# Kernel optimization log

Measured on AMD Instinct MI355X. Metric: run time of the kernel, lower is better.

Reference implementation:

```python
import jax, jax.numpy as jnp
import numpy as np

TEMPERATURE = 0.1
EPS_NORM = 1e-12  # torch F.normalize eps
EPS_LOSS = 1e-8


def setup_inputs() -> dict:
    key = jax.random.key(0)
    k1, k2 = jax.random.split(key)
    N, D, K = 8192, 512, 64
    features = jax.random.normal(k1, (N, D), dtype=jnp.float32)
    cluster_assignments = jax.random.randint(k2, (N,), 0, K, dtype=jnp.int64)
    return {"features": features, "cluster_assignments": cluster_assignments}


def reference(features, cluster_assignments):
    # L2 normalize rows (torch.nn.functional.normalize, p=2, dim=1)
    norm = jnp.linalg.norm(features, axis=1, keepdims=True)
    features_norm = features / jnp.maximum(norm, EPS_NORM)
    # pairwise cosine similarity scaled by temperature -> [N, N]
    sim = jnp.einsum('id,jd->ij', features_norm, features_norm) / TEMPERATURE
    exp_sim = jnp.exp(sim)
    mask = (cluster_assignments[None, :] == cluster_assignments[:, None]).astype(exp_sim.dtype)
    pos_sum = jnp.sum(exp_sim * mask, axis=1, keepdims=True)
    neg_sum = jnp.sum(exp_sim * (1.0 - mask), axis=1, keepdims=True)
    loss = -jnp.log(pos_sum / (pos_sum + neg_sum + EPS_LOSS))
    return jnp.sum(loss)  # reduction='sum'
```

## Files before the change

### kernel.cpp

```cpp
#include <hip/hip_runtime.h>
#include <hip/hip_bf16.h>
#include <stdint.h>

#define N 8192
#define D 512
#define TILE 128
#define NTB (N / TILE)
#define NBLK (NTB * (NTB + 1) / 2)
#define PANEL_BYTES (TILE * D)

typedef long long i64;
typedef __attribute__((ext_vector_type(4))) float f32x4;
typedef __attribute__((ext_vector_type(8))) int i32x8;

__global__ void cc_normalize(const float* __restrict__ F, uint8_t* __restrict__ Fn2,
                             float* __restrict__ out) {
    if (blockIdx.x == 0 && threadIdx.x == 0) out[0] = 0.0f;
    const int row  = blockIdx.x * 4 + (threadIdx.x >> 6);
    const int lane = threadIdx.x & 63;
    const float* p = F + (size_t)row * D + lane * 8;
    float4 a = *(const float4*)p;
    float4 b = *(const float4*)(p + 4);
    float ss = a.x*a.x + a.y*a.y + a.z*a.z + a.w*a.w
             + b.x*b.x + b.y*b.y + b.z*b.z + b.w*b.w;
    #pragma unroll
    for (int m = 32; m; m >>= 1) ss += __shfl_xor(ss, m, 64);
    const float inv = 16.0f / fmaxf(sqrtf(ss), 1e-12f);
    int lo = 0, hi = 0;
    lo = __builtin_amdgcn_cvt_pk_fp8_f32(a.x*inv, a.y*inv, lo, false);
    lo = __builtin_amdgcn_cvt_pk_fp8_f32(a.z*inv, a.w*inv, lo, true);
    hi = __builtin_amdgcn_cvt_pk_fp8_f32(b.x*inv, b.y*inv, hi, false);
    hi = __builtin_amdgcn_cvt_pk_fp8_f32(b.z*inv, b.w*inv, hi, true);
    const size_t idx = (size_t)(row >> 7) * PANEL_BYTES + (size_t)lane * 1024 + (row & 127) * 8;
    *(int2*)(Fn2 + idx) = make_int2(lo, hi);
}

__device__ __forceinline__ i32x8 load_frag(const uint8_t* p) {
    const int2 w0 = *(const int2*)(p);
    const int2 w1 = *(const int2*)(p + 1024);
    const int2 w2 = *(const int2*)(p + 2048);
    const int2 w3 = *(const int2*)(p + 3072);
    i32x8 v;
    v[0] = w0.x; v[1] = w0.y;
    v[2] = w1.x; v[3] = w1.y;
    v[4] = w2.x; v[5] = w2.y;
    v[6] = w3.x; v[7] = w3.y;
    return v;
}

#define MFMA128(A, B, C) __builtin_amdgcn_mfma_scale_f32_16x16x128_f8f6f4( \
    (A), (B), (C), 0, 0, 0, 0x7F7F7F7Fu, 0, 0x7F7F7F7Fu)

__global__ __launch_bounds__(256, 3)
void cc_gemm(const uint8_t* __restrict__ Fn2, const int* __restrict__ cl,
             float* __restrict__ Pt, float* __restrict__ Pp) {
    __shared__ int crow[TILE], ccol[TILE];
    __shared__ float2 rsum[2][TILE];
    __shared__ float2 csum[2][TILE];

    const int tid  = threadIdx.x;
    const int wave = tid >> 6;
    const int lane = tid & 63;

    int rem = blockIdx.x, bm = 0;
    while (rem >= NTB - bm) { rem -= NTB - bm; ++bm; }
    const int bn = bm + rem;
    const bool diag = (bm == bn);

    if (tid < TILE)            crow[tid]        = cl[bm * TILE + tid];
    else                       ccol[tid - TILE] = cl[bn * TILE + (tid - TILE)];

    const int wr = wave >> 1, wc = wave & 1;
    const int q   = lane >> 4;
    const int n15 = lane & 15;

    f32x4 acc[4][4];
    #pragma unroll
    for (int t = 0; t < 4; ++t)
        #pragma unroll
        for (int u = 0; u < 4; ++u) acc[t][u] = (f32x4)(0.0f);

    const int koff = (q >> 1) * 8192 + (q & 1) * 4096 + n15 * 8;
    const uint8_t* Ag = Fn2 + (size_t)bm * PANEL_BYTES + koff + (wr * 64) * 8;
    const uint8_t* Bg = Fn2 + (size_t)bn * PANEL_BYTES + koff + (wc * 64) * 8;

    #pragma unroll 1
    for (int c = 0; c < D / 128; ++c) {
        const uint8_t* pa = Ag + c * 16384;
        const uint8_t* pb = Bg + c * 16384;
        const i32x8 a0 = load_frag(pa);
        const i32x8 a1 = load_frag(pa + 128);
        const i32x8 a2 = load_frag(pa + 256);
        const i32x8 a3 = load_frag(pa + 384);
        const i32x8 b0 = load_frag(pb);
        const i32x8 b1 = load_frag(pb + 128);
        const i32x8 b2 = load_frag(pb + 256);
        const i32x8 b3 = load_frag(pb + 384);
        acc[0][0] = MFMA128(a0, b0, acc[0][0]);
        acc[0][1] = MFMA128(a0, b1, acc[0][1]);
        acc[0][2] = MFMA128(a0, b2, acc[0][2]);
        acc[0][3] = MFMA128(a0, b3, acc[0][3]);
        acc[1][0] = MFMA128(a1, b0, acc[1][0]);
        acc[1][1] = MFMA128(a1, b1, acc[1][1]);
        acc[1][2] = MFMA128(a1, b2, acc[1][2]);
        acc[1][3] = MFMA128(a1, b3, acc[1][3]);
        acc[2][0] = MFMA128(a2, b0, acc[2][0]);
        acc[2][1] = MFMA128(a2, b1, acc[2][1]);
        acc[2][2] = MFMA128(a2, b2, acc[2][2]);
        acc[2][3] = MFMA128(a2, b3, acc[2][3]);
        acc[3][0] = MFMA128(a3, b0, acc[3][0]);
        acc[3][1] = MFMA128(a3, b1, acc[3][1]);
        acc[3][2] = MFMA128(a3, b2, acc[3][2]);
        acc[3][3] = MFMA128(a3, b3, acc[3][3]);
    }

    __syncthreads();

    const float SC = 0.05635527503472514f;
    int cc[4];
    #pragma unroll
    for (int u = 0; u < 4; ++u) cc[u] = ccol[wc * 64 + u * 16 + n15];

    float ra[16], rp[16];
    float ce[4] = {0.f, 0.f, 0.f, 0.f};
    float cp2[4] = {0.f, 0.f, 0.f, 0.f};

    #pragma unroll
    for (int t = 0; t < 4; ++t) {
        #pragma unroll
        for (int r = 0; r < 4; ++r) {
            const int myc = crow[wr * 64 + t * 16 + q * 4 + r];
            float te = 0.0f, tp = 0.0f;
            #pragma unroll
            for (int u = 0; u < 4; ++u) {
                const float e  = exp2f(acc[t][u][r] * SC);
                const float ep = (cc[u] == myc) ? e : 0.0f;
                te += e;  tp += ep;
                ce[u] += e;  cp2[u] += ep;
            }
            ra[t * 4 + r] = te;  rp[t * 4 + r] = tp;
        }
    }

    {
        int len = 16;
        #pragma unroll
        for (int m = 1; m <= 8; m <<= 1) {
            const int half = len >> 1;
            const bool hiL = (lane & m) != 0;
            #pragma unroll
            for (int j = 0; j < half; ++j) {
                float sa = hiL ? ra[j] : ra[j + half];
                float sp = hiL ? rp[j] : rp[j + half];
                sa = __shfl_xor(sa, m, 64);
                sp = __shfl_xor(sp, m, 64);
                ra[j] = (hiL ? ra[j + half] : ra[j]) + sa;
                rp[j] = (hiL ? rp[j + half] : rp[j]) + sp;
            }
            len = half;
        }
        const int idx = ((n15 & 1) << 3) | ((n15 & 2) << 1) | ((n15 & 4) >> 1) | ((n15 & 8) >> 3);
        const int row = wr * 64 + (idx >> 2) * 16 + q * 4 + (idx & 3);
        rsum[wc][row] = make_float2(ra[0], rp[0]);
    }

    if (!diag) {
        int len = 4;
        #pragma unroll
        for (int m = 16; m <= 32; m <<= 1) {
            const int half = len >> 1;
            const bool hiL = (lane & m) != 0;
            #pragma unroll
            for (int j = 0; j < half; ++j) {
                float se = hiL ? ce[j] : ce[j + half];
                float sp = hiL ? cp2[j] : cp2[j + half];
                se = __shfl_xor(se, m, 64);
                sp = __shfl_xor(sp, m, 64);
                ce[j] = (hiL ? ce[j + half] : ce[j]) + se;
                cp2[j] = (hiL ? cp2[j + half] : cp2[j]) + sp;
            }
            len = half;
        }
        const int u = (((lane >> 4) & 1) << 1) | ((lane >> 5) & 1);
        const int col = wc * 64 + u * 16 + n15;
        csum[wr][col] = make_float2(ce[0], cp2[0]);
    }

    __syncthreads();
    if (tid < TILE) {
        const float2 r0 = rsum[0][tid], r1 = rsum[1][tid];
        const size_t o = (size_t)bn * N + bm * TILE + tid;
        Pt[o] = r0.x + r1.x;  Pp[o] = r0.y + r1.y;
    } else if (!diag) {
        const int c = tid - TILE;
        const float2 c0 = csum[0][c], c1 = csum[1][c];
        const size_t o = (size_t)bm * N + bn * TILE + c;
        Pt[o] = c0.x + c1.x;  Pp[o] = c0.y + c1.y;
    }
}

__global__ void cc_finalize(const float* __restrict__ Pt, const float* __restrict__ Pp,
                            float* __restrict__ out) {
    __shared__ float red[4];
    const int i = blockIdx.x * 256 + threadIdx.x;
    float tv = 0.0f, pv = 0.0f;
    #pragma unroll 8
    for (int s = 0; s < NTB; ++s) {
        tv += Pt[(size_t)s * N + i];
        pv += Pp[(size_t)s * N + i];
    }
    float l = __logf(tv + 1e-8f) - __logf(pv);
    #pragma unroll
    for (int m = 32; m; m >>= 1) l += __shfl_xor(l, m, 64);
    const int wv = threadIdx.x >> 6, lane = threadIdx.x & 63;
    if (lane == 0) red[wv] = l;
    __syncthreads();
    if (threadIdx.x == 0) atomicAdd(out, red[0] + red[1] + red[2] + red[3]);
}

extern "C" void kernel_launch(void* const* d_in, const int* in_sizes, int n_in,
                              void* d_out, int out_size, void* d_ws, size_t ws_size,
                              hipStream_t stream) {
    const float* F  = (const float*)d_in[0];
    const int*   cl = (const int*)d_in[1];
    float* out = (float*)d_out;

    uint8_t* Fn2 = (uint8_t*)d_ws;
    float* Pt  = (float*)((char*)d_ws + (size_t)N * D);
    float* Pp  = Pt + (size_t)NTB * N;

    cc_normalize<<<N / 4, 256, 0, stream>>>(F, Fn2, out);
    cc_gemm<<<NBLK, 256, 0, stream>>>(Fn2, cl, Pt, Pp);
    cc_finalize<<<N / 256, 256, 0, stream>>>(Pt, Pp, out);
}
```

Baseline: 116.9 us.

## Stage GEMM panels through double-buffered LDS with direct global-to-LDS loads

The FP8 GEMM kernel now copies each 16KB K-chunk of the A and B panels into shared memory using global_load_lds, double-buffered so the next chunk is prefetched while MFMAs run on the current one. Fragments are then read from LDS instead of straight from global memory, and the K loop is fully unrolled. This targets global-load latency and redundant per-wave global reads. In exchange it uses 64KB of LDS per block, lowers the launch-bounds occupancy hint from 3 to 2, and adds a barrier per chunk.

```diff
diff --git a/kernel.cpp b/kernel.cpp
--- a/kernel.cpp
+++ b/kernel.cpp
@@ -8,10 +8,17 @@
 #define NTB (N / TILE)
 #define NBLK (NTB * (NTB + 1) / 2)
 #define PANEL_BYTES (TILE * D)
+#define CHUNK 16384
 
 typedef long long i64;
 typedef __attribute__((ext_vector_type(4))) float f32x4;
 typedef __attribute__((ext_vector_type(8))) int i32x8;
+
+__device__ __forceinline__ void gload_lds16(const void* gp, const void* lp) {
+    auto g = (const __attribute__((address_space(1))) void*)(uintptr_t)gp;
+    auto l = (__attribute__((address_space(3))) void*)(uintptr_t)lp;
+    __builtin_amdgcn_global_load_lds(g, l, 16, 0, 0);
+}
 
 __global__ void cc_normalize(const float* __restrict__ F, uint8_t* __restrict__ Fn2,
                              float* __restrict__ out) {
@@ -35,7 +42,7 @@
     *(int2*)(Fn2 + idx) = make_int2(lo, hi);
 }
 
-__device__ __forceinline__ i32x8 load_frag(const uint8_t* p) {
+__device__ __forceinline__ i32x8 lds_frag(const uint8_t* p) {
     const int2 w0 = *(const int2*)(p);
     const int2 w1 = *(const int2*)(p + 1024);
     const int2 w2 = *(const int2*)(p + 2048);
@@ -51,9 +58,11 @@
 #define MFMA128(A, B, C) __builtin_amdgcn_mfma_scale_f32_16x16x128_f8f6f4( \
     (A), (B), (C), 0, 0, 0, 0x7F7F7F7Fu, 0, 0x7F7F7F7Fu)
 
-__global__ __launch_bounds__(256, 3)
+__global__ __launch_bounds__(256, 2)
 void cc_gemm(const uint8_t* __restrict__ Fn2, const int* __restrict__ cl,
              float* __restrict__ Pt, float* __restrict__ Pp) {
+    __shared__ __align__(16) uint8_t As[2][CHUNK];
+    __shared__ __align__(16) uint8_t Bs[2][CHUNK];
     __shared__ int crow[TILE], ccol[TILE];
     __shared__ float2 rsum[2][TILE];
     __shared__ float2 csum[2][TILE];
@@ -80,22 +89,40 @@
         #pragma unroll
         for (int u = 0; u < 4; ++u) acc[t][u] = (f32x4)(0.0f);
 
-    const int koff = (q >> 1) * 8192 + (q & 1) * 4096 + n15 * 8;
-    const uint8_t* Ag = Fn2 + (size_t)bm * PANEL_BYTES + koff + (wr * 64) * 8;
-    const uint8_t* Bg = Fn2 + (size_t)bn * PANEL_BYTES + koff + (wc * 64) * 8;
-
-    #pragma unroll 1
+    const uint8_t* Agp = Fn2 + (size_t)bm * PANEL_BYTES;
+    const uint8_t* Bgp = Fn2 + (size_t)bn * PANEL_BYTES;
+
+    auto stage = [&](int c, int buf) {
+        const uint8_t* ga = Agp + c * CHUNK;
+        const uint8_t* gb = Bgp + c * CHUNK;
+        #pragma unroll
+        for (int i = 0; i < 4; ++i) {
+            const int off = (wave * 4 + i) * 1024;
+            gload_lds16(ga + off + lane * 16, &As[buf][off]);
+            gload_lds16(gb + off + lane * 16, &Bs[buf][off]);
+        }
+    };
+
+    const int foff  = (q >> 1) * 8192 + (q & 1) * 4096 + n15 * 8;
+    const int abase = foff + (wr * 64) * 8;
+    const int bbase = foff + (wc * 64) * 8;
+
+    stage(0, 0);
+    asm volatile("s_waitcnt vmcnt(0) lgkmcnt(0)\n\ts_barrier" ::: "memory");
+
+    #pragma unroll
     for (int c = 0; c < D / 128; ++c) {
-        const uint8_t* pa = Ag + c * 16384;
-        const uint8_t* pb = Bg + c * 16384;
-        const i32x8 a0 = load_frag(pa);
-        const i32x8 a1 = load_frag(pa + 128);
-        const i32x8 a2 = load_frag(pa + 256);
-        const i32x8 a3 = load_frag(pa + 384);
-        const i32x8 b0 = load_frag(pb);
-        const i32x8 b1 = load_frag(pb + 128);
-        const i32x8 b2 = load_frag(pb + 256);
-        const i32x8 b3 = load_frag(pb + 384);
+        if (c < 3) stage(c + 1, (c + 1) & 1);
+        const uint8_t* ab = &As[c & 1][abase];
+        const uint8_t* bb = &Bs[c & 1][bbase];
+        const i32x8 a0 = lds_frag(ab);
+        const i32x8 a1 = lds_frag(ab + 128);
+        const i32x8 a2 = lds_frag(ab + 256);
+        const i32x8 a3 = lds_frag(ab + 384);
+        const i32x8 b0 = lds_frag(bb);
+        const i32x8 b1 = lds_frag(bb + 128);
+        const i32x8 b2 = lds_frag(bb + 256);
+        const i32x8 b3 = lds_frag(bb + 384);
         acc[0][0] = MFMA128(a0, b0, acc[0][0]);
         acc[0][1] = MFMA128(a0, b1, acc[0][1]);
         acc[0][2] = MFMA128(a0, b2, acc[0][2]);
@@ -112,6 +139,8 @@
         acc[3][1] = MFMA128(a3, b1, acc[3][1]);
         acc[3][2] = MFMA128(a3, b2, acc[3][2]);
         acc[3][3] = MFMA128(a3, b3, acc[3][3]);
+        if (c < 3)
+            asm volatile("s_waitcnt vmcnt(0) lgkmcnt(0)\n\ts_barrier" ::: "memory");
     }
 
     __syncthreads();
```

After: 130.5 us. 1.12x slower.
